# Optimization experiments

Measured on AMD Instinct MI355X. Metric: run time of the kernel, lower is better.

## Reference

```python
import jax, jax.numpy as jnp
import numpy as np

C_IN, SEQ_LEN, N_KERNELS, KSS, KS_MAX, BATCH = 1, 512, 1000, [7, 9, 11], 11, 64


def setup_inputs() -> dict:
    rng = np.random.default_rng(0)
    ks_l, dil_l, pad_l, lout_l = [], [], [], []
    W = np.zeros((N_KERNELS, C_IN, KS_MAX), dtype=np.float32)
    for k in range(N_KERNELS):
        ks = int(rng.choice(KSS))
        d_f = 2.0 ** rng.uniform(0.0, np.log2((SEQ_LEN - 1) // (ks - 1)))
        pad = int((ks - 1) * d_f // 2) if rng.integers(2) == 1 else 0
        d = int(d_f)
        # torch passes padding=2*pad to Conv1d -> adds 2*pad on EACH side
        lout = SEQ_LEN + 4 * pad - d * (ks - 1)
        w = rng.standard_normal((1, C_IN, ks)).astype(np.float32)
        w -= w.mean()  # center like the original (global mean)
        W[k, :, :ks] = w[0]
        ks_l.append(ks); dil_l.append(d); pad_l.append(pad); lout_l.append(lout)
    dils = np.asarray(dil_l, dtype=np.int64)
    pads = np.asarray(pad_l, dtype=np.int64)
    l_out = np.asarray(lout_l, dtype=np.int32)
    max_L = int(l_out.max())
    t = np.arange(max_L)
    j = np.arange(KS_MAX)
    # raw input index for output position t, tap j of kernel k
    raw = t[None, None, :] - 2 * pads[:, None, None] + j[None, :, None] * dils[:, None, None]
    valid = (raw >= 0) & (raw < SEQ_LEN)  # zero-padding semantics
    idx = np.clip(raw, 0, SEQ_LEN - 1).astype(np.int32)
    bias = (2.0 * (rng.random(N_KERNELS) - 0.5)).astype(np.float32)
    key = jax.random.key(0)
    x = jax.random.normal(key, (BATCH, C_IN, SEQ_LEN), dtype=jnp.float32)
    return {
        "x": x,
        "weight": jnp.asarray(W),
        "bias": jnp.asarray(bias),
        "idx": jnp.asarray(idx),
        "valid": jnp.asarray(valid),
        "l_out": jnp.asarray(l_out),
    }


def _forward(x, weight, bias, idx, valid, l_out):
    B = x.shape[0]
    K, C, KS = weight.shape
    L = idx.shape[-1]
    validf = valid.astype(x.dtype)  # [K, KS, L]
    acc = jnp.zeros((B, K, L), dtype=x.dtype)
    for j in range(KS):  # fixed small tap loop; each kernel vectorized over K
        xg = x[:, :, idx[:, j, :]]  # [B, C, K, L] gather along time
        acc = acc + jnp.einsum("bckt,kc->bkt", xg, weight[:, :, j]) * validf[None, :, j, :]
    out = acc + bias[None, :, None]  # [B, K, L]
    tmask = jnp.arange(L)[None, :] < l_out[:, None]  # [K, L] valid output positions
    neg = jnp.finfo(x.dtype).min
    mx = jnp.max(jnp.where(tmask[None], out, neg), axis=-1)  # [B, K]
    ppv = jnp.sum(jnp.where(tmask[None] & (out > 0), 1.0, 0.0), axis=-1) / l_out.astype(x.dtype)[None]
    # torch interleaves [max_i, ppv_i] along dim=1
    return jnp.stack([mx, ppv], axis=-1).reshape(B, 2 * K)


def reference(x, weight, bias, idx, valid, l_out):
    return _forward(x, weight, bias, idx, valid, l_out)
```

## Files before the change

kernel.cpp:

```cpp
#include <hip/hip_runtime.h>
#include <hip/hip_fp16.h>
#include <float.h>

constexpr int KMAX  = 11;
constexpr int SEQ   = 512;
constexpr int NB    = 64;
constexpr int NBB   = 8;
constexpr int NGRP  = NB / NBB;
constexpr int KPB   = 4;
constexpr int MSTR  = 32;
constexpr int X0    = 64;
constexpr int WSLOT = 640;

__device__ __forceinline__ unsigned h2b(__half2 h) { unsigned u; __builtin_memcpy(&u, &h, 4); return u; }
__device__ __forceinline__ __half2  b2h(unsigned u) { __half2 h; __builtin_memcpy(&h, &u, 4); return h; }

__device__ __forceinline__ unsigned pkmax(unsigned a, unsigned b) {
    unsigned d; asm("v_pk_max_f16 %0, %1, %2" : "=v"(d) : "v"(a), "v"(b)); return d;
}
__device__ __forceinline__ unsigned pkadd(unsigned a, unsigned b) { return h2b(__hadd2(b2h(a), b2h(b))); }
__device__ __forceinline__ __half2 h2max(__half2 a, __half2 b) { return b2h(pkmax(h2b(a), h2b(b))); }
__device__ __forceinline__ unsigned pkfma_clamp(unsigned a, unsigned b, unsigned c) {
    unsigned d; asm("v_pk_fma_f16 %0, %1, %2, %3 clamp" : "=v"(d) : "v"(a), "v"(b), "v"(c)); return d;
}

template<int CTRL>
__device__ __forceinline__ unsigned dppmov(unsigned old, unsigned v) {
    return (unsigned)__builtin_amdgcn_update_dpp((int)old, (int)v, CTRL, 0xF, 0xF, false);
}
constexpr unsigned NEGINF2 = 0xFC00FC00u;

__device__ __forceinline__ unsigned dpp_redmax(unsigned x) {
    x = pkmax(x, dppmov<0xB1 >(NEGINF2, x));
    x = pkmax(x, dppmov<0x4E >(NEGINF2, x));
    x = pkmax(x, dppmov<0x141>(NEGINF2, x));
    x = pkmax(x, dppmov<0x140>(NEGINF2, x));
    x = pkmax(x, dppmov<0x142>(NEGINF2, x));
    x = pkmax(x, dppmov<0x143>(NEGINF2, x));
    return x;
}
__device__ __forceinline__ unsigned dpp_redadd(unsigned x) {
    x = pkadd(x, dppmov<0xB1 >(0u, x));
    x = pkadd(x, dppmov<0x4E >(0u, x));
    x = pkadd(x, dppmov<0x141>(0u, x));
    x = pkadd(x, dppmov<0x140>(0u, x));
    x = pkadd(x, dppmov<0x142>(0u, x));
    x = pkadd(x, dppmov<0x143>(0u, x));
    return x;
}

__global__ __launch_bounds__(256)
void prep_kernel(const float* __restrict__ x, const float* __restrict__ w,
                 const int* __restrict__ idx, int* __restrict__ meta,
                 unsigned short* __restrict__ xt, int K, int maxL)
{
    const int tid = threadIdx.x;
    if ((int)blockIdx.x >= K) {
        const int j  = ((int)blockIdx.x - K) * 256 + tid;
        const int b  = j >> 7, s4 = j & 127;
        const float4 v = reinterpret_cast<const float4*>(x)[b * (SEQ / 4) + s4];
        const int g = b >> 3, bl = b & 7;
        unsigned short* dst = xt + ((size_t)g * SEQ + s4 * 4) * NBB + bl;
        __half h;
        h = __float2half_rn(v.x); __builtin_memcpy(&dst[0 * NBB], &h, 2);
        h = __float2half_rn(v.y); __builtin_memcpy(&dst[1 * NBB], &h, 2);
        h = __float2half_rn(v.z); __builtin_memcpy(&dst[2 * NBB], &h, 2);
        h = __float2half_rn(v.w); __builtin_memcpy(&dst[3 * NBB], &h, 2);
        return;
    }

    __shared__ int c_sh[KMAX];
    const int k = blockIdx.x, wave = tid >> 6, lane = tid & 63;
    const int tprobe = min(lane * 16, maxL - 1);

    int vv[3] = {0, 0, 0};
#pragma unroll
    for (int i = 0; i < 3; ++i) {
        const int j = wave + i * 4;
        if (j < KMAX) vv[i] = idx[((size_t)k * KMAX + j) * (size_t)maxL + tprobe];
    }
#pragma unroll
    for (int i = 0; i < 3; ++i) {
        const int j = wave + i * 4;
        if (j < KMAX) {
            int c = 0;
            const bool interior = (vv[i] > 0) && (vv[i] < SEQ - 1);
            const unsigned long long mb = __ballot(interior);
            if (mb != 0ull) {
                const int fl = __builtin_ctzll(mb);
                c = __shfl(vv[i], fl) - min(fl * 16, maxL - 1);
            } else {
                const int* row = idx + ((size_t)k * KMAX + j) * (size_t)maxL;
                for (int base = 0; base < maxL; base += 64) {
                    const int t2 = base + lane;
                    const int v2 = (t2 < maxL) ? row[t2] : 0;
                    const bool in2 = (v2 > 0) && (v2 < SEQ - 1);
                    const unsigned long long mb2 = __ballot(in2);
                    if (mb2 != 0ull) {
                        const int fl2 = __builtin_ctzll(mb2);
                        c = __shfl(v2, fl2) - (base + fl2);
                        break;
                    }
                }
            }
            if (lane == 0) c_sh[j] = c;
        }
    }
    __syncthreads();

    if (tid == 0) {
        int* mk = meta + (size_t)k * MSTR;
        int n = 0;
        for (int j = 0; j < KMAX; ++j) {
            const float wj = w[(size_t)k * KMAX + j];
            if (wj != 0.0f) {
                mk[1 + n] = c_sh[j];
                __half hw = __float2half_rn(wj);
                unsigned short ub; __builtin_memcpy(&ub, &hw, 2);
                mk[12 + n] = (unsigned)ub | ((unsigned)ub << 16);
                ++n;
            }
        }
        for (int jj = n; jj < KMAX; ++jj) { mk[1 + jj] = 1 << 20; mk[12 + jj] = 0; }
        mk[0] = n;
    }
}

template<int NJ>
__device__ __forceinline__ void conv_wave(
    const char* __restrict__ xsc, int mrow, int lout, int lane, unsigned ctermb,
    unsigned (&um)[4], unsigned (&uc)[4])
{
    const __half2 zero2 = __float2half2_rn(0.f);
    const __half2 nbig2 = __float2half2_rn(-65504.f);
    const unsigned C4b  = 0x74007400u;

    int addr[NJ], cs[NJ]; __half2 wr[NJ];
#pragma unroll
    for (int j = 0; j < NJ; ++j) {
        cs[j]   = __builtin_amdgcn_readlane(mrow, 1 + j);
        wr[j]   = b2h((unsigned)__builtin_amdgcn_readlane(mrow, 12 + j));
        addr[j] = (lane + cs[j] + X0) * 16;
    }
    __half2 mx2[4], ct2[4];
#pragma unroll
    for (int m = 0; m < 4; ++m) { mx2[m] = nbig2; ct2[m] = zero2; }

    const int nfull = lout >> 6;
    const int ng4   = nfull >> 2;

    for (int g = 0; g < ng4; ++g) {
        const int gb = g * 256;
#pragma unroll
        for (int u = 0; u < 4; ++u) {
            const int tb = gb + u * 64;
            __half2 a[4] = {zero2, zero2, zero2, zero2};
#pragma unroll
            for (int j = 0; j < NJ; ++j) {
                if ((unsigned)(tb + cs[j] + 63) < 575u) {
                    const uint4 d = *reinterpret_cast<const uint4*>(xsc + addr[j] + u * 1024);
                    a[0] = __hfma2(wr[j], b2h(d.x), a[0]);
                    a[1] = __hfma2(wr[j], b2h(d.y), a[1]);
                    a[2] = __hfma2(wr[j], b2h(d.z), a[2]);
                    a[3] = __hfma2(wr[j], b2h(d.w), a[3]);
                }
            }
#pragma unroll
            for (int m = 0; m < 4; ++m) {
                mx2[m] = h2max(mx2[m], a[m]);
                ct2[m] = b2h(pkadd(h2b(ct2[m]), pkfma_clamp(h2b(a[m]), C4b, ctermb)));
            }
        }
#pragma unroll
        for (int j = 0; j < NJ; ++j) addr[j] += 4096;
    }
    for (int u = 0; u < (nfull & 3); ++u) {
        const int tb = ng4 * 256 + u * 64;
        __half2 a[4] = {zero2, zero2, zero2, zero2};
#pragma unroll
        for (int j = 0; j < NJ; ++j) {
            if ((unsigned)(tb + cs[j] + 63) < 575u) {
                const uint4 d = *reinterpret_cast<const uint4*>(xsc + addr[j]);
                a[0] = __hfma2(wr[j], b2h(d.x), a[0]);
                a[1] = __hfma2(wr[j], b2h(d.y), a[1]);
                a[2] = __hfma2(wr[j], b2h(d.z), a[2]);
                a[3] = __hfma2(wr[j], b2h(d.w), a[3]);
            }
        }
#pragma unroll
        for (int m = 0; m < 4; ++m) {
            mx2[m] = h2max(mx2[m], a[m]);
            ct2[m] = b2h(pkadd(h2b(ct2[m]), pkfma_clamp(h2b(a[m]), C4b, ctermb)));
        }
#pragma unroll
        for (int j = 0; j < NJ; ++j) addr[j] += 1024;
    }
    const int rem = lout & 63;
    if (rem) {
        const int tb = nfull * 64;
        __half2 a[4] = {zero2, zero2, zero2, zero2};
#pragma unroll
        for (int j = 0; j < NJ; ++j) {
            if ((unsigned)(tb + cs[j] + 63) < 575u) {
                const uint4 d = *reinterpret_cast<const uint4*>(xsc + addr[j]);
                a[0] = __hfma2(wr[j], b2h(d.x), a[0]);
                a[1] = __hfma2(wr[j], b2h(d.y), a[1]);
                a[2] = __hfma2(wr[j], b2h(d.z), a[2]);
                a[3] = __hfma2(wr[j], b2h(d.w), a[3]);
            }
        }
        const bool tm = lane < rem;
#pragma unroll
        for (int m = 0; m < 4; ++m) {
            a[m] = tm ? a[m] : nbig2;
            mx2[m] = h2max(mx2[m], a[m]);
            ct2[m] = b2h(pkadd(h2b(ct2[m]), pkfma_clamp(h2b(a[m]), C4b, ctermb)));
        }
    }

#pragma unroll
    for (int m = 0; m < 4; ++m) {
        um[m] = dpp_redmax(h2b(mx2[m]));
        uc[m] = dpp_redadd(h2b(ct2[m]));
    }
}

__global__ __launch_bounds__(256, 8)
void rocket_main(const unsigned short* __restrict__ xt, const int* __restrict__ meta,
                 const float* __restrict__ bias, const int* __restrict__ l_out,
                 float* __restrict__ out, int K)
{
    __shared__ __align__(16) unsigned xs_u[WSLOT * 4];

    const int kbase = (int)blockIdx.x * KPB;
    const int grp   = blockIdx.y;
    const int tid   = threadIdx.x;
    const int wave  = tid >> 6, lane = tid & 63;

    float4* xs4 = reinterpret_cast<float4*>(xs_u);
    if (tid < 2 * X0) {
        const int slot = (tid < X0) ? tid : tid + SEQ;
        xs4[slot] = make_float4(0.f, 0.f, 0.f, 0.f);
    }
    const float4* src = reinterpret_cast<const float4*>(xt + (size_t)grp * SEQ * NBB);
    xs4[X0 + tid]       = src[tid];
    xs4[X0 + 256 + tid] = src[256 + tid];
    __syncthreads();

    const int k = kbase + wave;
    if (k >= K) return;

    const int mrow  = meta[(size_t)k * MSTR + (lane & 31)];
    const int nj    = __builtin_amdgcn_readlane(mrow, 0);
    const int lout  = __builtin_amdgcn_readfirstlane(l_out[k]);
    const float biasf = __int_as_float(__builtin_amdgcn_readfirstlane(__float_as_int(bias[k])));
    const unsigned ctermb = h2b(__float2half2_rn(biasf * 16384.f));

    unsigned um[4], uc[4];
    const char* xsc = reinterpret_cast<const char*>(xs_u);
    if (nj <= 7)      conv_wave<7 >(xsc, mrow, lout, lane, ctermb, um, uc);
    else if (nj <= 9) conv_wave<9 >(xsc, mrow, lout, lane, ctermb, um, uc);
    else              conv_wave<11>(xsc, mrow, lout, lane, ctermb, um, uc);

    if (lane == 63) {
        const float loutf = (float)lout;
#pragma unroll
        for (int m = 0; m < 4; ++m) {
            const __half2 hm = b2h(um[m]);
            const __half2 hc = b2h(uc[m]);
            float* o0 = out + (size_t)(grp * NBB + 2 * m) * (2 * K) + 2 * k;
            o0[0] = __low2float(hm) + biasf;
            o0[1] = __low2float(hc) / loutf;
            float* o1 = o0 + 2 * K;
            o1[0] = __high2float(hm) + biasf;
            o1[1] = __high2float(hc) / loutf;
        }
    }
}

extern "C" void kernel_launch(void* const* d_in, const int* in_sizes, int n_in,
                              void* d_out, int out_size, void* d_ws, size_t ws_size,
                              hipStream_t stream)
{
    const float* x    = (const float*)d_in[0];
    const float* w    = (const float*)d_in[1];
    const float* bias = (const float*)d_in[2];
    const int*   idx  = (const int*)d_in[3];
    const int*   lout = (const int*)d_in[5];
    float* out = (float*)d_out;

    const int K    = in_sizes[2];
    const int maxL = in_sizes[3] / (K * KMAX);

    int* meta = (int*)d_ws;
    size_t meta_bytes = ((size_t)K * MSTR * sizeof(int) + 255) & ~(size_t)255;
    unsigned short* xt = (unsigned short*)((char*)d_ws + meta_bytes);

    prep_kernel<<<K + 32, 256, 0, stream>>>(x, w, idx, meta, xt, K, maxL);
    rocket_main<<<dim3((K + KPB - 1) / KPB, NGRP), 256, 0, stream>>>(xt, meta, bias, lout, out, K);
}
```

Baseline: 34.48 us.

## Hoist per-tap guard over four output chunks with wider zero-padded LDS window

The shared-memory input window grows to 320 zero-padding slots on each side, so one bounds check per tap can cover four consecutive 64-position chunks. The tap loop is restructured: each tap issues four loads at fixed offsets and accumulates into a 4x4 array of accumulators, which removes per-chunk guards and per-tap address registers. LDS use per block goes from about 10 KB to 17 KB, which may limit occupancy, and the extra accumulators raise register pressure. The fallback shift constant becomes 1<<20 so that taps that are entirely out of range skip their loads.

```diff
diff --git a/kernel.cpp b/kernel.cpp
--- a/kernel.cpp
+++ b/kernel.cpp
@@ -9,8 +9,8 @@
 constexpr int NGRP  = NB / NBB;
 constexpr int KPB   = 4;
 constexpr int MSTR  = 32;
-constexpr int X0    = 64;
-constexpr int WSLOT = 640;
+constexpr int X0    = 320;
+constexpr int WSLOT = 1088;
 
 __device__ __forceinline__ unsigned h2b(__half2 h) { unsigned u; __builtin_memcpy(&u, &h, 4); return u; }
 __device__ __forceinline__ __half2  b2h(unsigned u) { __half2 h; __builtin_memcpy(&h, &u, 4); return h; }
@@ -83,7 +83,7 @@
     for (int i = 0; i < 3; ++i) {
         const int j = wave + i * 4;
         if (j < KMAX) {
-            int c = 0;
+            int c = 1 << 20;
             const bool interior = (vv[i] > 0) && (vv[i] < SEQ - 1);
             const unsigned long long mb = __ballot(interior);
             if (mb != 0ull) {
@@ -135,13 +135,14 @@
     const __half2 nbig2 = __float2half2_rn(-65504.f);
     const unsigned C4b  = 0x74007400u;
 
-    int addr[NJ], cs[NJ]; __half2 wr[NJ];
+    int cs[NJ]; unsigned wb[NJ];
 #pragma unroll
     for (int j = 0; j < NJ; ++j) {
-        cs[j]   = __builtin_amdgcn_readlane(mrow, 1 + j);
-        wr[j]   = b2h((unsigned)__builtin_amdgcn_readlane(mrow, 12 + j));
-        addr[j] = (lane + cs[j] + X0) * 16;
-    }
+        cs[j] = __builtin_amdgcn_readlane(mrow, 1 + j);
+        wb[j] = (unsigned)__builtin_amdgcn_readlane(mrow, 12 + j);
+    }
+    const int basev = (lane + X0) * 16;
+
     __half2 mx2[4], ct2[4];
 #pragma unroll
     for (int m = 0; m < 4; ++m) { mx2[m] = nbig2; ct2[m] = zero2; }
@@ -150,41 +151,64 @@
     const int ng4   = nfull >> 2;
 
     for (int g = 0; g < ng4; ++g) {
-        const int gb = g * 256;
+        const int tbg = g << 8;
+        __half2 a[4][4];
+#pragma unroll
+        for (int u = 0; u < 4; ++u)
+#pragma unroll
+            for (int m = 0; m < 4; ++m) a[u][m] = zero2;
+
+#pragma unroll
+        for (int j = 0; j < NJ; ++j) {
+            const int sc = tbg + cs[j];
+            if ((unsigned)(sc + 319) < 831u) {
+                const char* p = xsc + (basev + sc * 16);
+                const uint4 d0 = *reinterpret_cast<const uint4*>(p);
+                const uint4 d1 = *reinterpret_cast<const uint4*>(p + 1024);
+                const uint4 d2 = *reinterpret_cast<const uint4*>(p + 2048);
+                const uint4 d3 = *reinterpret_cast<const uint4*>(p + 3072);
+                const __half2 w2 = b2h(wb[j]);
+                a[0][0] = __hfma2(w2, b2h(d0.x), a[0][0]);
+                a[0][1] = __hfma2(w2, b2h(d0.y), a[0][1]);
+                a[0][2] = __hfma2(w2, b2h(d0.z), a[0][2]);
+                a[0][3] = __hfma2(w2, b2h(d0.w), a[0][3]);
+                a[1][0] = __hfma2(w2, b2h(d1.x), a[1][0]);
+                a[1][1] = __hfma2(w2, b2h(d1.y), a[1][1]);
+                a[1][2] = __hfma2(w2, b2h(d1.z), a[1][2]);
+                a[1][3] = __hfma2(w2, b2h(d1.w), a[1][3]);
+                a[2][0] = __hfma2(w2, b2h(d2.x), a[2][0]);
+                a[2][1] = __hfma2(w2, b2h(d2.y), a[2][1]);
+                a[2][2] = __hfma2(w2, b2h(d2.z), a[2][2]);
+                a[2][3] = __hfma2(w2, b2h(d2.w), a[2][3]);
+                a[3][0] = __hfma2(w2, b2h(d3.x), a[3][0]);
+                a[3][1] = __hfma2(w2, b2h(d3.y), a[3][1]);
+                a[3][2] = __hfma2(w2, b2h(d3.z), a[3][2]);
+                a[3][3] = __hfma2(w2, b2h(d3.w), a[3][3]);
+            }
+        }
 #pragma unroll
         for (int u = 0; u < 4; ++u) {
-            const int tb = gb + u * 64;
-            __half2 a[4] = {zero2, zero2, zero2, zero2};
-#pragma unroll
-            for (int j = 0; j < NJ; ++j) {
-                if ((unsigned)(tb + cs[j] + 63) < 575u) {
-                    const uint4 d = *reinterpret_cast<const uint4*>(xsc + addr[j] + u * 1024);
-                    a[0] = __hfma2(wr[j], b2h(d.x), a[0]);
-                    a[1] = __hfma2(wr[j], b2h(d.y), a[1]);
-                    a[2] = __hfma2(wr[j], b2h(d.z), a[2]);
-                    a[3] = __hfma2(wr[j], b2h(d.w), a[3]);
-                }
-            }
 #pragma unroll
             for (int m = 0; m < 4; ++m) {
-                mx2[m] = h2max(mx2[m], a[m]);
-                ct2[m] = b2h(pkadd(h2b(ct2[m]), pkfma_clamp(h2b(a[m]), C4b, ctermb)));
-            }
-        }
-#pragma unroll
-        for (int j = 0; j < NJ; ++j) addr[j] += 4096;
-    }
+                mx2[m] = h2max(mx2[m], a[u][m]);
+                ct2[m] = b2h(pkadd(h2b(ct2[m]), pkfma_clamp(h2b(a[u][m]), C4b, ctermb)));
+            }
+        }
+    }
+
     for (int u = 0; u < (nfull & 3); ++u) {
-        const int tb = ng4 * 256 + u * 64;
+        const int tb = (ng4 << 8) + (u << 6);
         __half2 a[4] = {zero2, zero2, zero2, zero2};
 #pragma unroll
         for (int j = 0; j < NJ; ++j) {
-            if ((unsigned)(tb + cs[j] + 63) < 575u) {
-                const uint4 d = *reinterpret_cast<const uint4*>(xsc + addr[j]);
-                a[0] = __hfma2(wr[j], b2h(d.x), a[0]);
-                a[1] = __hfma2(wr[j], b2h(d.y), a[1]);
-                a[2] = __hfma2(wr[j], b2h(d.z), a[2]);
-                a[3] = __hfma2(wr[j], b2h(d.w), a[3]);
+            const int sc = tb + cs[j];
+            if ((unsigned)(sc + 63) < 575u) {
+                const uint4 d = *reinterpret_cast<const uint4*>(xsc + (basev + sc * 16));
+                const __half2 w2 = b2h(wb[j]);
+                a[0] = __hfma2(w2, b2h(d.x), a[0]);
+                a[1] = __hfma2(w2, b2h(d.y), a[1]);
+                a[2] = __hfma2(w2, b2h(d.z), a[2]);
+                a[3] = __hfma2(w2, b2h(d.w), a[3]);
             }
         }
 #pragma unroll
@@ -192,21 +216,22 @@
             mx2[m] = h2max(mx2[m], a[m]);
             ct2[m] = b2h(pkadd(h2b(ct2[m]), pkfma_clamp(h2b(a[m]), C4b, ctermb)));
         }
-#pragma unroll
-        for (int j = 0; j < NJ; ++j) addr[j] += 1024;
-    }
+    }
+
     const int rem = lout & 63;
     if (rem) {
-        const int tb = nfull * 64;
+        const int tb = nfull << 6;
         __half2 a[4] = {zero2, zero2, zero2, zero2};
 #pragma unroll
         for (int j = 0; j < NJ; ++j) {
-            if ((unsigned)(tb + cs[j] + 63) < 575u) {
-                const uint4 d = *reinterpret_cast<const uint4*>(xsc + addr[j]);
-                a[0] = __hfma2(wr[j], b2h(d.x), a[0]);
-                a[1] = __hfma2(wr[j], b2h(d.y), a[1]);
-                a[2] = __hfma2(wr[j], b2h(d.z), a[2]);
-                a[3] = __hfma2(wr[j], b2h(d.w), a[3]);
+            const int sc = tb + cs[j];
+            if ((unsigned)(sc + 63) < 575u) {
+                const uint4 d = *reinterpret_cast<const uint4*>(xsc + (basev + sc * 16));
+                const __half2 w2 = b2h(wb[j]);
+                a[0] = __hfma2(w2, b2h(d.x), a[0]);
+                a[1] = __hfma2(w2, b2h(d.y), a[1]);
+                a[2] = __hfma2(w2, b2h(d.z), a[2]);
+                a[3] = __hfma2(w2, b2h(d.w), a[3]);
             }
         }
         const bool tm = lane < rem;
@@ -238,13 +263,12 @@
     const int wave  = tid >> 6, lane = tid & 63;
 
     float4* xs4 = reinterpret_cast<float4*>(xs_u);
-    if (tid < 2 * X0) {
-        const int slot = (tid < X0) ? tid : tid + SEQ;
-        xs4[slot] = make_float4(0.f, 0.f, 0.f, 0.f);
-    }
     const float4* src = reinterpret_cast<const float4*>(xt + (size_t)grp * SEQ * NBB);
-    xs4[X0 + tid]       = src[tid];
-    xs4[X0 + 256 + tid] = src[256 + tid];
+    const float4 z4 = make_float4(0.f, 0.f, 0.f, 0.f);
+    for (int i = tid; i < WSLOT; i += 256) {
+        const int s = i - X0;
+        xs4[i] = ((unsigned)s < (unsigned)SEQ) ? src[s] : z4;
+    }
     __syncthreads();
 
     const int k = kbase + wave;
```

Result: slower. 37.77 us (+9.5%).
